# Kernel optimization log

Hardware: AMD Instinct MI355X
Metric: run time of the kernel (lower is better)

## Reference

```python
import jax, jax.numpy as jnp
import numpy as np

CODEBOOK_BITS = 8      # log2(256)
NUM_Q = 2              # NUM_QUANTIZERS
INV_TEMP = 100.0       # LFQ default inv_temperature
DIVERSITY_GAMMA = 1.0
ENTROPY_WEIGHT = 0.1   # LFQ default entropy_loss_weight
COMMIT_WEIGHT = 1.0


def conv2d(x, w, b, pad):
    out = jax.lax.conv_general_dilated(
        x, w, (1, 1), [(pad, pad), (pad, pad)],
        dimension_numbers=('NCHW', 'OIHW', 'NCHW'))
    return out + b[None, :, None, None]


def maxpool2(x):
    return jax.lax.reduce_window(x, -jnp.inf, jax.lax.max,
                                 (1, 1, 2, 2), (1, 1, 2, 2), 'VALID')


def groupnorm(x, groups=4, eps=1e-5):
    B, C, H, W = x.shape
    xg = x.reshape(B, groups, C // groups, H, W)
    mu = xg.mean(axis=(2, 3, 4), keepdims=True)
    var = xg.var(axis=(2, 3, 4), keepdims=True)
    return ((xg - mu) * jax.lax.rsqrt(var + eps)).reshape(B, C, H, W)


def upsample2(x):  # nearest, scale 2
    return jnp.repeat(jnp.repeat(x, 2, axis=2), 2, axis=3)


def lfq_codebook():
    # all 2^8 sign patterns, code j has bit i = ((j>>i)&1)*2-1
    j = jnp.arange(2 ** CODEBOOK_BITS)
    bits = ((j[:, None] >> jnp.arange(CODEBOOK_BITS)[None, :]) & 1).astype(jnp.float32)
    return bits * 2.0 - 1.0  # [256, 8]


def lfq_residual(z):
    # z: (B, D, H, W) with D = CODEBOOK_BITS
    codebook = lfq_codebook()
    t = jnp.transpose(z, (0, 2, 3, 1))  # (B,H,W,D) tokens
    residual = t
    quantized_out = jnp.zeros_like(t)
    pow2 = (2 ** jnp.arange(CODEBOOK_BITS)).astype(jnp.int32)
    indices = []
    aux = jnp.zeros((), t.dtype)
    for _ in range(NUM_Q):
        q_hard = jnp.where(residual > 0, 1.0, -1.0).astype(t.dtype)
        # straight-through binarization
        q = residual + jax.lax.stop_gradient(q_hard - residual)
        idx = jnp.sum((q_hard > 0).astype(jnp.int32) * pow2, axis=-1)  # (B,H,W)
        logits = (2.0 * INV_TEMP) * jnp.einsum('bhwd,cd->bhwc', residual, codebook)
        logp = jax.nn.log_softmax(logits, axis=-1)
        probs = jnp.exp(logp)
        per_sample_entropy = -jnp.mean(jnp.sum(probs * logp, axis=-1))
        avg_prob = jnp.mean(probs.reshape(-1, probs.shape[-1]), axis=0)
        codebook_entropy = -jnp.sum(avg_prob * jnp.log(avg_prob + 1e-10))
        entropy_aux = per_sample_entropy - DIVERSITY_GAMMA * codebook_entropy
        commit = jnp.mean((residual - jax.lax.stop_gradient(q_hard)) ** 2)
        aux = aux + ENTROPY_WEIGHT * entropy_aux + COMMIT_WEIGHT * commit
        quantized_out = quantized_out + q
        residual = residual - jax.lax.stop_gradient(q)
        indices.append(idx)
    q_out = jnp.transpose(quantized_out, (0, 3, 1, 2))  # (B,D,H,W)
    return q_out, jnp.stack(indices, axis=-1), aux


def setup_inputs() -> dict:
    key = jax.random.key(0)
    ks = jax.random.split(key, 13)
    s = 0.05
    return {
        'x': jax.random.normal(ks[0], (32, 1, 256, 256), jnp.float32),
        'w1': jax.random.normal(ks[1], (16, 1, 3, 3), jnp.float32) * s,
        'b1': jax.random.normal(ks[2], (16,), jnp.float32) * s,
        'w2': jax.random.normal(ks[3], (32, 16, 3, 3), jnp.float32) * s,
        'b2': jax.random.normal(ks[4], (32,), jnp.float32) * s,
        'w3': jax.random.normal(ks[5], (8, 32, 1, 1), jnp.float32) * s,
        'b3': jax.random.normal(ks[6], (8,), jnp.float32) * s,
        'd1': jax.random.normal(ks[7], (32, 8, 3, 3), jnp.float32) * s,
        'db1': jax.random.normal(ks[8], (32,), jnp.float32) * s,
        'd2': jax.random.normal(ks[9], (16, 32, 3, 3), jnp.float32) * s,
        'db2': jax.random.normal(ks[10], (16,), jnp.float32) * s,
        'd3': jax.random.normal(ks[11], (1, 16, 3, 3), jnp.float32) * s,
        'db3': jax.random.normal(ks[12], (1,), jnp.float32) * s,
    }


def reference(x, w1, b1, w2, b2, w3, b3, d1, db1, d2, db2, d3, db3):
    # encode
    h = jax.nn.gelu(maxpool2(conv2d(x, w1, b1, pad=1)), approximate=False)
    h = groupnorm(maxpool2(conv2d(h, w2, b2, pad=1)))
    h = conv2d(h, w3, b3, pad=0)  # (B,8,64,64)
    # residual LFQ
    q, indices, aux = lfq_residual(h)
    # decode
    y = upsample2(conv2d(q, d1, db1, pad=1))
    y = upsample2(jax.nn.gelu(conv2d(y, d2, db2, pad=1), approximate=False))
    y = conv2d(y, d3, db3, pad=1)
    return jnp.clip(y, -1.0, 1.0), indices, aux
```

## Files before the change

### kernel.cpp

```cpp
#include <hip/hip_runtime.h>
#include <hip/hip_bf16.h>
#include <math.h>

#define DEV __device__ __forceinline__

DEV float gelu_exact(float x){ return 0.5f*x*(1.0f + erff(x*0.70710678118654752f)); }

__global__ __launch_bounds__(256) void k_conv1(const float* __restrict__ x,
    const float* __restrict__ w1, const float* __restrict__ b1,
    float* __restrict__ h1,
    const float* __restrict__ w2, const float* __restrict__ d2,
    float* __restrict__ w2t, float* __restrict__ wp4d2)
{
  __shared__ float sE[34*19], sO[34*19];
  const int b = blockIdx.z;
  const int r0 = blockIdx.x*32, c0 = blockIdx.y*32;
  const float* xp = x + (size_t)b*65536;
  for(int i=threadIdx.x;i<34*34;i+=256){
    int r=i/34, c=i-r*34;
    int gr=r0+r-1, gc=c0+c-1;
    float v=0.f;
    if(gr>=0 && gr<256 && gc>=0 && gc<256) v = xp[gr*256+gc];
    if(c&1) sO[r*19+(c>>1)]=v; else sE[r*19+(c>>1)]=v;
  }
  __syncthreads();
  const int tx=threadIdx.x&15, ty=threadIdx.x>>4;
  const int base = 2*ty*19 + tx;
  float in[4][4];
  #pragma unroll
  for(int r=0;r<4;r++){
    in[r][0]=sE[base+r*19]; in[r][1]=sO[base+r*19];
    in[r][2]=sE[base+r*19+1]; in[r][3]=sO[base+r*19+1];
  }
  const int py = blockIdx.x*16+ty, px = blockIdx.y*16+tx;
  float* op = h1 + ((size_t)b*16)*16384 + py*128 + px;
  #pragma unroll
  for(int ch=0;ch<16;ch++){
    float m=-1e30f;
    #pragma unroll
    for(int pr=0;pr<2;pr++)
      #pragma unroll
      for(int pc=0;pc<2;pc++){
        float a=0.f;
        #pragma unroll
        for(int ky=0;ky<3;ky++)
          #pragma unroll
          for(int kx=0;kx<3;kx++)
            a = fmaf(in[pr+ky][pc+kx], w1[ch*9+ky*3+kx], a);
        m = fmaxf(m,a);
      }
    op[(size_t)ch*16384] = gelu_exact(m + b1[ch]);
  }
  if(blockIdx.x==0 && blockIdx.y==0 && b<8){
    const int gid = b*256 + threadIdx.x;
    for(int i=gid;i<4608;i+=2048){
      int oc=i/144, rem=i-oc*144, ic=rem/9, k=rem-ic*9;
      w2t[(ic*32+oc)*9+k]=w2[i];
    }
    for(int i=gid;i<2048;i+=2048){
      int par=i>>9, ic=(i>>4)&31, oc=i&15;
      int pyp=par>>1, pxp=par&1;
      const float* wg = d2 + ((size_t)oc*32+ic)*9;
      float a00=0.f,a01=0.f,a10=0.f,a11=0.f;
      #pragma unroll
      for(int ky=0;ky<3;ky++){
        int sy = pyp ? (ky>>1) : ((ky>0)?1:0);
        #pragma unroll
        for(int kx=0;kx<3;kx++){
          int sx = pxp ? (kx>>1) : ((kx>0)?1:0);
          float wv=wg[ky*3+kx];
          if(sy==0){ if(sx==0)a00+=wv; else a01+=wv; }
          else     { if(sx==0)a10+=wv; else a11+=wv; }
        }
      }
      float* dst=wp4d2+(size_t)i*4;
      dst[0]=a00; dst[1]=a01; dst[2]=a10; dst[3]=a11;
    }
  }
}

__global__ __launch_bounds__(256) void k_conv2(const float* __restrict__ h1,
    const float* __restrict__ w2t, const float* __restrict__ b2,
    float* __restrict__ h2, double* __restrict__ pb)
{
  __shared__ __align__(16) float t2[2][8*360];
  const int b=blockIdx.z;
  const int r0=blockIdx.x*16, c0=blockIdx.y*16;
  const float* hp = h1 + (size_t)b*16*16384;
  const int t=threadIdx.x;
  int lofs[6]; int gof[6]; bool ok0[6], ok1[6];
  #pragma unroll
  for(int s=0;s<6;s++){
    int idx=s*256+t;
    int ic=idx/162, rem=idx-162*ic, lr=rem/9, jp=rem-9*lr;
    int gr=r0+lr-1, gc=c0+2*jp-1;
    bool rok = (gr>=0) && (gr<128);
    ok0[s] = rok && (gc>=0);
    ok1[s] = rok && (gc+1<128);
    lofs[s]= ic*360+lr*20+2*jp;
    gof[s] = ic*16384 + gr*128 + gc;
  }
  float a0[6], a1[6], c0r[6], c1r[6];
  #pragma unroll
  for(int s=0;s<6;s++){
    if(s<5 || t<16){
      a0[s] = ok0[s] ? hp[gof[s]]   : 0.f;
      a1[s] = ok1[s] ? hp[gof[s]+1] : 0.f;
    }
  }
  #pragma unroll
  for(int s=0;s<6;s++)
    if(s<5 || t<16) *(float2*)&t2[0][lofs[s]]=make_float2(a0[s],a1[s]);
  const float* hp1 = hp + 8*16384;
  #pragma unroll
  for(int s=0;s<6;s++){
    if(s<5 || t<16){
      c0r[s] = ok0[s] ? hp1[gof[s]]   : 0.f;
      c1r[s] = ok1[s] ? hp1[gof[s]+1] : 0.f;
    }
  }
  __syncthreads();

  const int pos=t&63;
  const int ocg=__builtin_amdgcn_readfirstlane((int)(t>>6));
  const int oc0=ocg*8;
  const int pyl=pos>>3, pxl=pos&7;
  const int base0 = 2*pyl*20 + 2*pxl;
  float acc[8][4];
  #pragma unroll
  for(int o=0;o<8;o++)
    #pragma unroll
    for(int j=0;j<4;j++) acc[o][j]=0.f;

  #pragma unroll 4
  for(int ic=0;ic<8;ic++){
    float in[4][4];
    #pragma unroll
    for(int r=0;r<4;r++){
      float2 a=*(const float2*)&t2[0][ic*360 + base0 + r*20];
      float2 c=*(const float2*)&t2[0][ic*360 + base0 + r*20 + 2];
      in[r][0]=a.x; in[r][1]=a.y; in[r][2]=c.x; in[r][3]=c.y;
    }
    const float* wp = w2t + (ic*32+oc0)*9;
    #pragma unroll
    for(int o=0;o<8;o++){
      #pragma unroll
      for(int pr=0;pr<2;pr++)
        #pragma unroll
        for(int pc=0;pc<2;pc++){
          float s=acc[o][pr*2+pc];
          #pragma unroll
          for(int ky=0;ky<3;ky++)
            #pragma unroll
            for(int kx=0;kx<3;kx++)
              s=fmaf(in[pr+ky][pc+kx], wp[o*9+ky*3+kx], s);
          acc[o][pr*2+pc]=s;
        }
    }
  }
  #pragma unroll
  for(int s=0;s<6;s++)
    if(s<5 || t<16) *(float2*)&t2[1][lofs[s]]=make_float2(c0r[s],c1r[s]);
  __syncthreads();
  #pragma unroll 4
  for(int ic=0;ic<8;ic++){
    float in[4][4];
    #pragma unroll
    for(int r=0;r<4;r++){
      float2 a=*(const float2*)&t2[1][ic*360 + base0 + r*20];
      float2 c=*(const float2*)&t2[1][ic*360 + base0 + r*20 + 2];
      in[r][0]=a.x; in[r][1]=a.y; in[r][2]=c.x; in[r][3]=c.y;
    }
    const float* wp = w2t + ((8+ic)*32+oc0)*9;
    #pragma unroll
    for(int o=0;o<8;o++){
      #pragma unroll
      for(int pr=0;pr<2;pr++)
        #pragma unroll
        for(int pc=0;pc<2;pc++){
          float s=acc[o][pr*2+pc];
          #pragma unroll
          for(int ky=0;ky<3;ky++)
            #pragma unroll
            for(int kx=0;kx<3;kx++)
              s=fmaf(in[pr+ky][pc+kx], wp[o*9+ky*3+kx], s);
          acc[o][pr*2+pc]=s;
        }
    }
  }

  const int py=blockIdx.x*8+pyl, px=blockIdx.y*8+pxl;
  double s=0.0, s2=0.0;
  #pragma unroll
  for(int o=0;o<8;o++){
    const int oc=oc0+o;
    float m=fmaxf(fmaxf(acc[o][0],acc[o][1]),fmaxf(acc[o][2],acc[o][3]));
    float hv=m+b2[oc];
    h2[(((size_t)b*32+oc)*64+py)*64+px]=hv;
    s += (double)hv; s2 += (double)hv*(double)hv;
  }
  #pragma unroll
  for(int off=32;off;off>>=1){
    s  += __shfl_xor(s,  off, 64);
    s2 += __shfl_xor(s2, off, 64);
  }
  if(pos==0){
    const int bidx = blockIdx.x*8 + blockIdx.y;
    double* p = pb + (((size_t)b*4+ocg)*64 + bidx)*2;
    p[0]=s; p[1]=s2;
  }
}

__global__ __launch_bounds__(256) void k_lfq(const float* __restrict__ h2,
    const double* __restrict__ pb, const float* __restrict__ w3, const float* __restrict__ b3,
    float* __restrict__ qout, float* __restrict__ idxout,
    float* __restrict__ avgp, float* __restrict__ ec)
{
  __shared__ __align__(16) float tabL[16*260];
  __shared__ __align__(16) float tabH[16*260];
  __shared__ float smu[4], srs[4];
  const int blk=blockIdx.x;
  const int b=blk>>4;
  const int t=threadIdx.x;
  const int h=(blk&15)*4 + (t>>6);
  const int w=t&63;
  {
    const int wv=t>>6, ln=t&63;
    double s = pb[(((size_t)b*4+wv)*64+ln)*2];
    double s2= pb[(((size_t)b*4+wv)*64+ln)*2+1];
    #pragma unroll
    for(int off=32;off;off>>=1){
      s  += __shfl_xor(s,  off, 64);
      s2 += __shfl_xor(s2, off, 64);
    }
    if(ln==0){
      double mu=s/32768.0;
      double var=s2/32768.0 - mu*mu;
      smu[wv]=(float)mu;
      srs[wv]=(float)(1.0/sqrt(var+1e-5));
    }
  }
  __syncthreads();
  float mu[4], rs[4];
  #pragma unroll
  for(int g=0;g<4;g++){ mu[g]=smu[g]; rs[g]=srs[g]; }
  const float* hp = h2 + (size_t)b*131072 + h*64 + w;
  float z[8];
  #pragma unroll
  for(int d=0;d<8;d++) z[d]=b3[d];
  #pragma unroll
  for(int c=0;c<32;c++){
    float xn=(hp[(size_t)c*4096]-mu[c>>3])*rs[c>>3];
    #pragma unroll
    for(int d=0;d<8;d++) z[d]=fmaf(xn, w3[d*32+c], z[d]);
  }
  float r[8], qsum[8];
  #pragma unroll
  for(int d=0;d<8;d++){ r[d]=z[d]; qsum[d]=0.f; }
  float entk[2], comk[2];
  #pragma unroll
  for(int k=0;k<2;k++){
    int idx=0; float ent=0.f, com=0.f;
    float pb0[8], pb1[8];
    #pragma unroll
    for(int d=0;d<8;d++){
      float rv=r[d];
      bool pos = rv>0.f;
      float sgn = pos?1.f:-1.f;
      idx |= (pos?1:0)<<d;
      float dd=rv-sgn; com=fmaf(dd,dd,com);
      float a=400.f*fabsf(rv);
      float e=__expf(-a);
      float p=1.f/(1.f+e);
      ent += a - p*a - __logf(p);
      float pm=p, pq=1.f-p;
      pb1[d]=pos?pm:pq;
      pb0[d]=pos?pq:pm;
      qsum[d]+=sgn;
      r[d]=rv-sgn;
    }
    float lo[16], hi[16];
    lo[0]=pb0[0]; lo[1]=pb1[0];
    lo[2]=lo[0]*pb1[1]; lo[3]=lo[1]*pb1[1]; lo[0]*=pb0[1]; lo[1]*=pb0[1];
    lo[4]=lo[0]*pb1[2]; lo[5]=lo[1]*pb1[2]; lo[6]=lo[2]*pb1[2]; lo[7]=lo[3]*pb1[2];
    lo[0]*=pb0[2]; lo[1]*=pb0[2]; lo[2]*=pb0[2]; lo[3]*=pb0[2];
    lo[8]=lo[0]*pb1[3]; lo[9]=lo[1]*pb1[3]; lo[10]=lo[2]*pb1[3]; lo[11]=lo[3]*pb1[3];
    lo[12]=lo[4]*pb1[3]; lo[13]=lo[5]*pb1[3]; lo[14]=lo[6]*pb1[3]; lo[15]=lo[7]*pb1[3];
    lo[0]*=pb0[3]; lo[1]*=pb0[3]; lo[2]*=pb0[3]; lo[3]*=pb0[3];
    lo[4]*=pb0[3]; lo[5]*=pb0[3]; lo[6]*=pb0[3]; lo[7]*=pb0[3];
    hi[0]=pb0[4]; hi[1]=pb1[4];
    hi[2]=hi[0]*pb1[5]; hi[3]=hi[1]*pb1[5]; hi[0]*=pb0[5]; hi[1]*=pb0[5];
    hi[4]=hi[0]*pb1[6]; hi[5]=hi[1]*pb1[6]; hi[6]=hi[2]*pb1[6]; hi[7]=hi[3]*pb1[6];
    hi[0]*=pb0[6]; hi[1]*=pb0[6]; hi[2]*=pb0[6]; hi[3]*=pb0[6];
    hi[8]=hi[0]*pb1[7]; hi[9]=hi[1]*pb1[7]; hi[10]=hi[2]*pb1[7]; hi[11]=hi[3]*pb1[7];
    hi[12]=hi[4]*pb1[7]; hi[13]=hi[5]*pb1[7]; hi[14]=hi[6]*pb1[7]; hi[15]=hi[7]*pb1[7];
    hi[0]*=pb0[7]; hi[1]*=pb0[7]; hi[2]*=pb0[7]; hi[3]*=pb0[7];
    hi[4]*=pb0[7]; hi[5]*=pb0[7]; hi[6]*=pb0[7]; hi[7]*=pb0[7];
    #pragma unroll
    for(int m=0;m<16;m++){ tabL[m*260+t]=lo[m]; tabH[m*260+t]=hi[m]; }
    __syncthreads();
    float accp=0.f, accq=0.f;
    const int jl=t&15, jh=t>>4;
    const float* Lp=&tabL[jl*260];
    const float* Hp=&tabH[jh*260];
    #pragma unroll 4
    for(int q4=0;q4<64;q4++){
      float4 L=*(const float4*)&Lp[4*q4];
      float4 H=*(const float4*)&Hp[4*q4];
      accp=fmaf(L.x,H.x,accp); accq=fmaf(L.y,H.y,accq);
      accp=fmaf(L.z,H.z,accp); accq=fmaf(L.w,H.w,accq);
    }
    avgp[((size_t)k*512+blk)*256+t]=accp+accq;
    __syncthreads();
    entk[k]=ent; comk[k]=com;
    idxout[((size_t)(b*64+h)*64+w)*2+k]=(float)idx;
  }
  #pragma unroll
  for(int d=0;d<8;d++)
    qout[(((size_t)b*8+d)*64+h)*64+w]=qsum[d];
  tabL[t]=entk[0]; tabL[256+t]=entk[1]; tabL[512+t]=comk[0]; tabL[768+t]=comk[1];
  __syncthreads();
  for(int st=128;st>0;st>>=1){
    if(t<st){ tabL[t]+=tabL[t+st]; tabL[256+t]+=tabL[256+t+st];
              tabL[512+t]+=tabL[512+t+st]; tabL[768+t]+=tabL[768+t+st]; }
    __syncthreads();
  }
  if(t==0){ ec[blk*4+0]=tabL[0]; ec[blk*4+1]=tabL[256]; ec[blk*4+2]=tabL[512]; ec[blk*4+3]=tabL[768]; }
}

__global__ __launch_bounds__(256) void k_red(const float* __restrict__ avgp,
    float* __restrict__ avgs)
{
  const int k=blockIdx.x>>4, c0=(blockIdx.x&15)*16;
  const int col=threadIdx.x&15, rg=threadIdx.x>>4;
  float s=0.f;
  for(int j=0;j<32;j++){
    int blk=rg+16*j;
    s+=avgp[((size_t)k*512+blk)*256+c0+col];
  }
  __shared__ float red[256];
  red[threadIdx.x]=s; __syncthreads();
  for(int st=128;st>=16;st>>=1){
    if(threadIdx.x<st) red[threadIdx.x]+=red[threadIdx.x+st];
    __syncthreads();
  }
  if(threadIdx.x<16) avgs[k*256+c0+threadIdx.x]=red[threadIdx.x];
}

__global__ __launch_bounds__(256) void k_final(const float* __restrict__ avgs,
    const float* __restrict__ ec, float* __restrict__ auxout)
{
  __shared__ double red[256];
  const int t=threadIdx.x;
  double cb=0.0;
  #pragma unroll
  for(int k=0;k<2;k++){
    double ap=(double)avgs[k*256+t]*(1.0/131072.0);
    cb += -(ap*log(ap+1e-10));
  }
  red[t]=cb; __syncthreads();
  for(int st=128;st>0;st>>=1){ if(t<st) red[t]+=red[t+st]; __syncthreads(); }
  double CB=red[0]; __syncthreads();
  double e=0.0,c=0.0;
  for(int blk=t;blk<512;blk+=256){
    e += (double)ec[blk*4+0]+(double)ec[blk*4+1];
    c += (double)ec[blk*4+2]+(double)ec[blk*4+3];
  }
  red[t]=e; __syncthreads();
  for(int st=128;st>0;st>>=1){ if(t<st) red[t]+=red[t+st]; __syncthreads(); }
  double E=red[0]; __syncthreads();
  red[t]=c; __syncthreads();
  for(int st=128;st>0;st>>=1){ if(t<st) red[t]+=red[t+st]; __syncthreads(); }
  if(t==0){
    double C=red[0];
    double aux = 0.1*(E*(1.0/131072.0) - CB) + C*(1.0/1048576.0);
    auxout[0]=(float)aux;
  }
}

__global__ __launch_bounds__(256) void k_dec1(const float* __restrict__ q,
    const float* __restrict__ d1, const float* __restrict__ db1, float* __restrict__ out1)
{
  __shared__ float tile[8*110];
  const int b=blockIdx.z, r0=blockIdx.x*8, c0=blockIdx.y*8;
  const float* qp = q + (size_t)b*8*4096;
  for(int i=threadIdx.x;i<800;i+=256){
    int ic=i/100, rem=i-ic*100, r=rem/10, c=rem-r*10;
    int gr=r0+r-1, gc=c0+c-1;
    float v=0.f;
    if(gr>=0&&gr<64&&gc>=0&&gc<64) v=qp[ic*4096+gr*64+gc];
    tile[ic*110+r*11+c]=v;
  }
  __syncthreads();
  const int ocg=__builtin_amdgcn_readfirstlane((int)(threadIdx.x>>6));
  const int oc0=ocg*8;
  const int l=threadIdx.x&63, ry=l>>3, cx=l&7;
  float acc[8];
  #pragma unroll
  for(int o=0;o<8;o++) acc[o]=db1[oc0+o];
  #pragma unroll 2
  for(int ic=0;ic<8;ic++){
    float v[9];
    #pragma unroll
    for(int ky=0;ky<3;ky++)
      #pragma unroll
      for(int kx=0;kx<3;kx++)
        v[ky*3+kx]=tile[ic*110+(ry+ky)*11+cx+kx];
    #pragma unroll
    for(int o=0;o<8;o++){
      const float* wp=&d1[((oc0+o)*8+ic)*9];
      float s=acc[o];
      #pragma unroll
      for(int kk=0;kk<9;kk++) s=fmaf(v[kk],wp[kk],s);
      acc[o]=s;
    }
  }
  #pragma unroll
  for(int o=0;o<8;o++)
    out1[(((size_t)b*32+oc0+o)*64 + r0+ry)*64 + c0+cx]=acc[o];
}

__global__ __launch_bounds__(256) void k_dec2(const float* __restrict__ out1,
    const float* __restrict__ wp4d2, const float* __restrict__ db2, float* __restrict__ out2)
{
  __shared__ float tile[32*110];
  const int b=blockIdx.z, y0=blockIdx.x*16, x0=blockIdx.y*16;
  const int sy0=(y0>>1)-1, sx0=(x0>>1)-1;
  const float* sp = out1 + (size_t)b*32*4096;
  for(int i=threadIdx.x;i<3200;i+=256){
    int ic=i/100, rem=i-ic*100, r=rem/10, c=rem-r*10;
    int gr=sy0+r, gc=sx0+c;
    float v=0.f;
    if(gr>=0&&gr<64&&gc>=0&&gc<64) v=sp[ic*4096+gr*64+gc];
    tile[ic*110+r*11+c]=v;
  }
  __syncthreads();
  const int par=__builtin_amdgcn_readfirstlane((int)(threadIdx.x>>6));
  const int py=par>>1, px=par&1;
  const int l=threadIdx.x&63, ry=l>>3, cx=l&7;
  const int byl=ry+py, bxl=cx+px;
  float acc[16];
  #pragma unroll
  for(int o=0;o<16;o++) acc[o]=db2[o];
  #pragma unroll 2
  for(int ic=0;ic<32;ic++){
    const float* tp=&tile[ic*110 + byl*11 + bxl];
    const float s00=tp[0], s01=tp[1], s10=tp[11], s11=tp[12];
    const float* wq = wp4d2 + (size_t)((par*32+ic)*16)*4;
    #pragma unroll
    for(int o=0;o<16;o++)
      acc[o]=fmaf(s00,wq[o*4],fmaf(s01,wq[o*4+1],fmaf(s10,wq[o*4+2],fmaf(s11,wq[o*4+3],acc[o]))));
  }
  const int Y=y0+2*ry+py, X=x0+2*cx+px;
  #pragma unroll
  for(int o=0;o<16;o++)
    out2[((size_t)b*16+o)*16384 + (size_t)Y*128 + X] = gelu_exact(acc[o]);
}

__global__ __launch_bounds__(256) void k_dec3(const float* __restrict__ out2,
    const float* __restrict__ d3, const float* __restrict__ db3, float* __restrict__ y)
{
  __shared__ float tile[16*342];
  __shared__ float4 wp4[64];
  const int b=blockIdx.z, y0=blockIdx.x*32, x0=blockIdx.y*32;
  const int sy0=(y0>>1)-1, sx0=(x0>>1)-1;
  const float* sp = out2 + (size_t)b*16*16384;
  for(int i=threadIdx.x;i<16*324;i+=256){
    int ic=i/324, rem=i-ic*324, r=rem/18, c=rem-r*18;
    int gr=sy0+r, gc=sx0+c;
    float v=0.f;
    if(gr>=0&&gr<128&&gc>=0&&gc<128) v=sp[ic*16384+gr*128+gc];
    tile[ic*342+r*19+c]=v;
  }
  if(threadIdx.x<64){
    int par=threadIdx.x>>4, ic=threadIdx.x&15;
    int py=par>>1, px=par&1;
    const float* wg = d3 + ic*9;
    float a00=0.f,a01=0.f,a10=0.f,a11=0.f;
    #pragma unroll
    for(int ky=0;ky<3;ky++){
      int sy = py ? (ky>>1) : ((ky>0)?1:0);
      #pragma unroll
      for(int kx=0;kx<3;kx++){
        int sx = px ? (kx>>1) : ((kx>0)?1:0);
        float wv=wg[ky*3+kx];
        if(sy==0){ if(sx==0)a00+=wv; else a01+=wv; }
        else     { if(sx==0)a10+=wv; else a11+=wv; }
      }
    }
    wp4[threadIdx.x]=make_float4(a00,a01,a10,a11);
  }
  __syncthreads();
  const float bias=db3[0];
  const int par=__builtin_amdgcn_readfirstlane((int)(threadIdx.x>>6));
  const int py=par>>1, px=par&1;
  const int l=threadIdx.x&63, r0l=l>>4, cl=l&15;
  const int bxl=cl+px;
  float acc[4];
  #pragma unroll
  for(int a=0;a<4;a++) acc[a]=bias;
  #pragma unroll 2
  for(int ic=0;ic<16;ic++){
    const float4 wv=wp4[par*16+ic];
    #pragma unroll
    for(int a=0;a<4;a++){
      const int byl=r0l+4*a+py;
      const float* tp=&tile[ic*342 + byl*19 + bxl];
      acc[a]=fmaf(tp[0],wv.x,fmaf(tp[1],wv.y,fmaf(tp[19],wv.z,fmaf(tp[20],wv.w,acc[a]))));
    }
  }
  #pragma unroll
  for(int a=0;a<4;a++){
    const int yy=2*(r0l+4*a)+py, xx=2*cl+px;
    float v=fminf(fmaxf(acc[a],-1.0f),1.0f);
    y[(size_t)b*65536 + (size_t)(y0+yy)*256 + (x0+xx)] = v;
  }
}

extern "C" void kernel_launch(void* const* d_in, const int* in_sizes, int n_in,
                              void* d_out, int out_size, void* d_ws, size_t ws_size,
                              hipStream_t stream)
{
  const float* x  =(const float*)d_in[0];
  const float* w1 =(const float*)d_in[1];
  const float* b1 =(const float*)d_in[2];
  const float* w2 =(const float*)d_in[3];
  const float* b2 =(const float*)d_in[4];
  const float* w3 =(const float*)d_in[5];
  const float* b3 =(const float*)d_in[6];
  const float* d1 =(const float*)d_in[7];
  const float* db1=(const float*)d_in[8];
  const float* d2 =(const float*)d_in[9];
  const float* db2=(const float*)d_in[10];
  const float* d3 =(const float*)d_in[11];
  const float* db3=(const float*)d_in[12];
  float* out=(float*)d_out;
  float* ws =(float*)d_ws;
  float* h1   = ws;
  float* h2   = ws + 8388608;
  float* qb   = ws + 12582912;
  float* avgp = ws + 13631744;
  float* ec   = ws + 13893888;
  float* wp4d2= ws + 13895936;
  float* avgs = ws + 13904128;
  float* w2t  = avgp;
  double* pb  = (double*)out;
  float* out1 = h2;
  float* out2 = h1;

  k_conv1<<<dim3(8,8,32),256,0,stream>>>(x,w1,b1,h1,w2,d2,w2t,wp4d2);
  k_conv2<<<dim3(8,8,32),256,0,stream>>>(h1,w2t,b2,h2,pb);
  k_lfq  <<<dim3(512),256,0,stream>>>(h2,pb,w3,b3,qb,out+2097152,avgp,ec);
  k_red  <<<dim3(32),256,0,stream>>>(avgp,avgs);
  k_final<<<dim3(1),256,0,stream>>>(avgs,ec,out+2359296);
  k_dec1 <<<dim3(8,8,32),256,0,stream>>>(qb,d1,db1,out1);
  k_dec2 <<<dim3(8,8,32),256,0,stream>>>(out1,wp4d2,db2,out2);
  k_dec3 <<<dim3(8,8,32),256,0,stream>>>(out2,d3,db3,out);
}
```

Measured before the change: 194.3 us.

## Fuse three decoder convolutions and avg-prob reduction into one tiled kernel

Merges dec1, dec2 and dec3 into one kernel that keeps the intermediate feature maps in shared memory per 32x32 output tile, computing the halos redundantly. The goal is to avoid writing and reading the 32-channel and 16-channel intermediates through global memory and to save three launches. The k_red reduction is folded into a subset of the decoder blocks. The cost is recomputing the halo regions, heavier shared memory use that may lower occupancy, and a small load imbalance on the blocks that also reduce.

```diff
diff --git a/kernel.cpp b/kernel.cpp
--- a/kernel.cpp
+++ b/kernel.cpp
@@ -328,23 +328,171 @@
   if(t==0){ ec[blk*4+0]=tabL[0]; ec[blk*4+1]=tabL[256]; ec[blk*4+2]=tabL[512]; ec[blk*4+3]=tabL[768]; }
 }
 
-__global__ __launch_bounds__(256) void k_red(const float* __restrict__ avgp,
-    float* __restrict__ avgs)
+__global__ __launch_bounds__(256) void k_dec(const float* __restrict__ q,
+    const float* __restrict__ d1, const float* __restrict__ db1,
+    const float* __restrict__ wp4d2, const float* __restrict__ db2,
+    const float* __restrict__ d3, const float* __restrict__ db3,
+    float* __restrict__ y,
+    const float* __restrict__ avgp, float* __restrict__ avgs)
 {
-  const int k=blockIdx.x>>4, c0=(blockIdx.x&15)*16;
-  const int col=threadIdx.x&15, rg=threadIdx.x>>4;
-  float s=0.f;
-  for(int j=0;j<32;j++){
-    int blk=rg+16*j;
-    s+=avgp[((size_t)k*512+blk)*256+c0+col];
-  }
+  __shared__ float o1[32*110];
+  __shared__ float o2[16*342];
+  __shared__ float4 wp4[64];
   __shared__ float red[256];
-  red[threadIdx.x]=s; __syncthreads();
-  for(int st=128;st>=16;st>>=1){
-    if(threadIdx.x<st) red[threadIdx.x]+=red[threadIdx.x+st];
-    __syncthreads();
-  }
-  if(threadIdx.x<16) avgs[k*256+c0+threadIdx.x]=red[threadIdx.x];
+  const int b=blockIdx.z, bx=blockIdx.x, by=blockIdx.y;
+  const int t=threadIdx.x;
+  float* qs = o2;
+
+  const float* qp = q + (size_t)b*8*4096;
+  const int qr0=8*bx-2, qc0=8*by-2;
+  for(int i=t;i<1152;i+=256){
+    int ic=i/144, rem=i-144*ic, r=rem/12, c=rem-12*r;
+    int gr=qr0+r, gc=qc0+c;
+    float v=0.f;
+    if((unsigned)gr<64u && (unsigned)gc<64u) v=qp[ic*4096+gr*64+gc];
+    qs[ic*156+r*13+c]=v;
+  }
+  if(t<64){
+    int par=t>>4, ic=t&15;
+    int pyp=par>>1, pxp=par&1;
+    const float* wg = d3 + ic*9;
+    float a00=0.f,a01=0.f,a10=0.f,a11=0.f;
+    #pragma unroll
+    for(int ky=0;ky<3;ky++){
+      int sy = pyp ? (ky>>1) : ((ky>0)?1:0);
+      #pragma unroll
+      for(int kx=0;kx<3;kx++){
+        int sx = pxp ? (kx>>1) : ((kx>0)?1:0);
+        float wv=wg[ky*3+kx];
+        if(sy==0){ if(sx==0)a00+=wv; else a01+=wv; }
+        else     { if(sx==0)a10+=wv; else a11+=wv; }
+      }
+    }
+    wp4[t]=make_float4(a00,a01,a10,a11);
+  }
+  __syncthreads();
+
+  {
+    const int wv=__builtin_amdgcn_readfirstlane((int)(t>>6));
+    const int oc0=wv*8;
+    const int l=t&63;
+    #pragma unroll
+    for(int s=0;s<2;s++){
+      int j=l+64*s;
+      if(j<100){
+        int r=j/10, c=j-10*r;
+        bool valid = ((unsigned)(8*bx-1+r)<64u) && ((unsigned)(8*by-1+c)<64u);
+        float acc[8];
+        #pragma unroll
+        for(int o=0;o<8;o++) acc[o]=db1[oc0+o];
+        if(valid){
+          #pragma unroll 2
+          for(int ic=0;ic<8;ic++){
+            float v[9];
+            #pragma unroll
+            for(int ky=0;ky<3;ky++)
+              #pragma unroll
+              for(int kx=0;kx<3;kx++)
+                v[ky*3+kx]=qs[ic*156+(r+ky)*13+(c+kx)];
+            #pragma unroll
+            for(int o=0;o<8;o++){
+              const float* wp=&d1[((oc0+o)*8+ic)*9];
+              float ss=acc[o];
+              #pragma unroll
+              for(int kk=0;kk<9;kk++) ss=fmaf(v[kk],wp[kk],ss);
+              acc[o]=ss;
+            }
+          }
+        }
+        #pragma unroll
+        for(int o=0;o<8;o++)
+          o1[(oc0+o)*110 + r*11 + c] = valid ? acc[o] : 0.f;
+      }
+    }
+  }
+  __syncthreads();
+
+  {
+    const int wv=__builtin_amdgcn_readfirstlane((int)(t>>6));
+    const int ocb=wv*4;
+    const int l=t&63;
+    #pragma unroll
+    for(int par4=0;par4<4;par4++){
+      const int qr=par4>>1, qc=par4&1;
+      const int par=((qr^1)<<1)|(qc^1);
+      const float* wqb = wp4d2 + (size_t)(par*512)*4;
+      #pragma unroll
+      for(int s=0;s<2;s++){
+        int j=l+64*s;
+        if(j<81){
+          int rq=j/9, cq=j-9*rq;
+          int rr=2*rq+qr, cc=2*cq+qc;
+          bool valid = ((unsigned)(16*bx-1+rr)<128u)&&((unsigned)(16*by-1+cc)<128u);
+          float acc[4];
+          #pragma unroll
+          for(int o=0;o<4;o++) acc[o]=db2[ocb+o];
+          #pragma unroll 4
+          for(int ic=0;ic<32;ic++){
+            const float* tp=&o1[ic*110 + rq*11 + cq];
+            float s00=tp[0], s01=tp[1], s10=tp[11], s11=tp[12];
+            const float* wq = wqb + (ic*16+ocb)*4;
+            #pragma unroll
+            for(int o=0;o<4;o++)
+              acc[o]=fmaf(s00,wq[o*4],fmaf(s01,wq[o*4+1],fmaf(s10,wq[o*4+2],fmaf(s11,wq[o*4+3],acc[o]))));
+          }
+          #pragma unroll
+          for(int o=0;o<4;o++)
+            o2[(ocb+o)*342 + rr*19 + cc] = valid ? gelu_exact(acc[o]) : 0.f;
+        }
+      }
+    }
+  }
+  __syncthreads();
+
+  {
+    const float bias=db3[0];
+    const int par=__builtin_amdgcn_readfirstlane((int)(t>>6));
+    const int py=par>>1, px=par&1;
+    const int l=t&63, r0l=l>>4, cl=l&15;
+    const int bxl=cl+px;
+    float acc[4];
+    #pragma unroll
+    for(int a=0;a<4;a++) acc[a]=bias;
+    #pragma unroll 2
+    for(int ic=0;ic<16;ic++){
+      const float4 wv4=wp4[par*16+ic];
+      #pragma unroll
+      for(int a=0;a<4;a++){
+        const int byl=r0l+4*a+py;
+        const float* tp=&o2[ic*342 + byl*19 + bxl];
+        acc[a]=fmaf(tp[0],wv4.x,fmaf(tp[1],wv4.y,fmaf(tp[19],wv4.z,fmaf(tp[20],wv4.w,acc[a]))));
+      }
+    }
+    const int y0=bx*32, x0=by*32;
+    #pragma unroll
+    for(int a=0;a<4;a++){
+      const int yy=2*(r0l+4*a)+py, xx=2*cl+px;
+      float v=fminf(fmaxf(acc[a],-1.0f),1.0f);
+      y[(size_t)b*65536 + (size_t)(y0+yy)*256 + (x0+xx)] = v;
+    }
+  }
+
+  if(bx==0 && b<4){
+    const int rid = b*8 + by;
+    const int k=rid>>4, cc0=(rid&15)*16;
+    const int col=t&15, rg=t>>4;
+    float s=0.f;
+    for(int j=0;j<32;j++){
+      int blk=rg+16*j;
+      s+=avgp[((size_t)k*512+blk)*256+cc0+col];
+    }
+    red[t]=s; __syncthreads();
+    for(int st=128;st>=16;st>>=1){
+      if(t<st) red[t]+=red[t+st];
+      __syncthreads();
+    }
+    if(t<16) avgs[k*256+cc0+t]=red[t];
+  }
 }
 
 __global__ __launch_bounds__(256) void k_final(const float* __restrict__ avgs,
@@ -375,145 +523,6 @@
     double C=red[0];
     double aux = 0.1*(E*(1.0/131072.0) - CB) + C*(1.0/1048576.0);
     auxout[0]=(float)aux;
-  }
-}
-
-__global__ __launch_bounds__(256) void k_dec1(const float* __restrict__ q,
-    const float* __restrict__ d1, const float* __restrict__ db1, float* __restrict__ out1)
-{
-  __shared__ float tile[8*110];
-  const int b=blockIdx.z, r0=blockIdx.x*8, c0=blockIdx.y*8;
-  const float* qp = q + (size_t)b*8*4096;
-  for(int i=threadIdx.x;i<800;i+=256){
-    int ic=i/100, rem=i-ic*100, r=rem/10, c=rem-r*10;
-    int gr=r0+r-1, gc=c0+c-1;
-    float v=0.f;
-    if(gr>=0&&gr<64&&gc>=0&&gc<64) v=qp[ic*4096+gr*64+gc];
-    tile[ic*110+r*11+c]=v;
-  }
-  __syncthreads();
-  const int ocg=__builtin_amdgcn_readfirstlane((int)(threadIdx.x>>6));
-  const int oc0=ocg*8;
-  const int l=threadIdx.x&63, ry=l>>3, cx=l&7;
-  float acc[8];
-  #pragma unroll
-  for(int o=0;o<8;o++) acc[o]=db1[oc0+o];
-  #pragma unroll 2
-  for(int ic=0;ic<8;ic++){
-    float v[9];
-    #pragma unroll
-    for(int ky=0;ky<3;ky++)
-      #pragma unroll
-      for(int kx=0;kx<3;kx++)
-        v[ky*3+kx]=tile[ic*110+(ry+ky)*11+cx+kx];
-    #pragma unroll
-    for(int o=0;o<8;o++){
-      const float* wp=&d1[((oc0+o)*8+ic)*9];
-      float s=acc[o];
-      #pragma unroll
-      for(int kk=0;kk<9;kk++) s=fmaf(v[kk],wp[kk],s);
-      acc[o]=s;
-    }
-  }
-  #pragma unroll
-  for(int o=0;o<8;o++)
-    out1[(((size_t)b*32+oc0+o)*64 + r0+ry)*64 + c0+cx]=acc[o];
-}
-
-__global__ __launch_bounds__(256) void k_dec2(const float* __restrict__ out1,
-    const float* __restrict__ wp4d2, const float* __restrict__ db2, float* __restrict__ out2)
-{
-  __shared__ float tile[32*110];
-  const int b=blockIdx.z, y0=blockIdx.x*16, x0=blockIdx.y*16;
-  const int sy0=(y0>>1)-1, sx0=(x0>>1)-1;
-  const float* sp = out1 + (size_t)b*32*4096;
-  for(int i=threadIdx.x;i<3200;i+=256){
-    int ic=i/100, rem=i-ic*100, r=rem/10, c=rem-r*10;
-    int gr=sy0+r, gc=sx0+c;
-    float v=0.f;
-    if(gr>=0&&gr<64&&gc>=0&&gc<64) v=sp[ic*4096+gr*64+gc];
-    tile[ic*110+r*11+c]=v;
-  }
-  __syncthreads();
-  const int par=__builtin_amdgcn_readfirstlane((int)(threadIdx.x>>6));
-  const int py=par>>1, px=par&1;
-  const int l=threadIdx.x&63, ry=l>>3, cx=l&7;
-  const int byl=ry+py, bxl=cx+px;
-  float acc[16];
-  #pragma unroll
-  for(int o=0;o<16;o++) acc[o]=db2[o];
-  #pragma unroll 2
-  for(int ic=0;ic<32;ic++){
-    const float* tp=&tile[ic*110 + byl*11 + bxl];
-    const float s00=tp[0], s01=tp[1], s10=tp[11], s11=tp[12];
-    const float* wq = wp4d2 + (size_t)((par*32+ic)*16)*4;
-    #pragma unroll
-    for(int o=0;o<16;o++)
-      acc[o]=fmaf(s00,wq[o*4],fmaf(s01,wq[o*4+1],fmaf(s10,wq[o*4+2],fmaf(s11,wq[o*4+3],acc[o]))));
-  }
-  const int Y=y0+2*ry+py, X=x0+2*cx+px;
-  #pragma unroll
-  for(int o=0;o<16;o++)
-    out2[((size_t)b*16+o)*16384 + (size_t)Y*128 + X] = gelu_exact(acc[o]);
-}
-
-__global__ __launch_bounds__(256) void k_dec3(const float* __restrict__ out2,
-    const float* __restrict__ d3, const float* __restrict__ db3, float* __restrict__ y)
-{
-  __shared__ float tile[16*342];
-  __shared__ float4 wp4[64];
-  const int b=blockIdx.z, y0=blockIdx.x*32, x0=blockIdx.y*32;
-  const int sy0=(y0>>1)-1, sx0=(x0>>1)-1;
-  const float* sp = out2 + (size_t)b*16*16384;
-  for(int i=threadIdx.x;i<16*324;i+=256){
-    int ic=i/324, rem=i-ic*324, r=rem/18, c=rem-r*18;
-    int gr=sy0+r, gc=sx0+c;
-    float v=0.f;
-    if(gr>=0&&gr<128&&gc>=0&&gc<128) v=sp[ic*16384+gr*128+gc];
-    tile[ic*342+r*19+c]=v;
-  }
-  if(threadIdx.x<64){
-    int par=threadIdx.x>>4, ic=threadIdx.x&15;
-    int py=par>>1, px=par&1;
-    const float* wg = d3 + ic*9;
-    float a00=0.f,a01=0.f,a10=0.f,a11=0.f;
-    #pragma unroll
-    for(int ky=0;ky<3;ky++){
-      int sy = py ? (ky>>1) : ((ky>0)?1:0);
-      #pragma unroll
-      for(int kx=0;kx<3;kx++){
-        int sx = px ? (kx>>1) : ((kx>0)?1:0);
-        float wv=wg[ky*3+kx];
-        if(sy==0){ if(sx==0)a00+=wv; else a01+=wv; }
-        else     { if(sx==0)a10+=wv; else a11+=wv; }
-      }
-    }
-    wp4[threadIdx.x]=make_float4(a00,a01,a10,a11);
-  }
-  __syncthreads();
-  const float bias=db3[0];
-  const int par=__builtin_amdgcn_readfirstlane((int)(threadIdx.x>>6));
-  const int py=par>>1, px=par&1;
-  const int l=threadIdx.x&63, r0l=l>>4, cl=l&15;
-  const int bxl=cl+px;
-  float acc[4];
-  #pragma unroll
-  for(int a=0;a<4;a++) acc[a]=bias;
-  #pragma unroll 2
-  for(int ic=0;ic<16;ic++){
-    const float4 wv=wp4[par*16+ic];
-    #pragma unroll
-    for(int a=0;a<4;a++){
-      const int byl=r0l+4*a+py;
-      const float* tp=&tile[ic*342 + byl*19 + bxl];
-      acc[a]=fmaf(tp[0],wv.x,fmaf(tp[1],wv.y,fmaf(tp[19],wv.z,fmaf(tp[20],wv.w,acc[a]))));
-    }
-  }
-  #pragma unroll
-  for(int a=0;a<4;a++){
-    const int yy=2*(r0l+4*a)+py, xx=2*cl+px;
-    float v=fminf(fmaxf(acc[a],-1.0f),1.0f);
-    y[(size_t)b*65536 + (size_t)(y0+yy)*256 + (x0+xx)] = v;
   }
 }
 
@@ -545,15 +554,10 @@
   float* avgs = ws + 13904128;
   float* w2t  = avgp;
   double* pb  = (double*)out;
-  float* out1 = h2;
-  float* out2 = h1;
 
   k_conv1<<<dim3(8,8,32),256,0,stream>>>(x,w1,b1,h1,w2,d2,w2t,wp4d2);
   k_conv2<<<dim3(8,8,32),256,0,stream>>>(h1,w2t,b2,h2,pb);
   k_lfq  <<<dim3(512),256,0,stream>>>(h2,pb,w3,b3,qb,out+2097152,avgp,ec);
-  k_red  <<<dim3(32),256,0,stream>>>(avgp,avgs);
+  k_dec  <<<dim3(8,8,32),256,0,stream>>>(qb,d1,db1,wp4d2,db2,d3,db3,out,avgp,avgs);
   k_final<<<dim3(1),256,0,stream>>>(avgs,ec,out+2359296);
-  k_dec1 <<<dim3(8,8,32),256,0,stream>>>(qb,d1,db1,out1);
-  k_dec2 <<<dim3(8,8,32),256,0,stream>>>(out1,wp4d2,db2,out2);
-  k_dec3 <<<dim3(8,8,32),256,0,stream>>>(out2,d3,db3,out);
 }
```

Measured after the change: 224.5 us. +15.6%, slower.
